# Performance work log

Measured on AMD Instinct MI355X. Metric: run time of the kernel, lower is better.

Reference implementation:

```python
import jax, jax.numpy as jnp
import numpy as np

B, T, C, H, R = 2, 2048, 2048, 16, 8
D = C // H  # head_dim = 128


def _rope_cache(seq_len, dim, theta=10000.0):
    pos = jnp.arange(seq_len, dtype=jnp.float32)[:, None]            # [T,1]
    idx = jnp.arange(0, dim, 2, dtype=jnp.float32)                   # [D/2]
    freqs = 1.0 / (theta ** (idx / dim))
    ang = pos * freqs                                                # [T, D/2]
    return jnp.cos(ang), jnp.sin(ang)


def setup_inputs() -> dict:
    key = jax.random.key(0)
    ks = jax.random.split(key, 16)
    s = 0.02
    inp = {"x": jax.random.normal(ks[0], (B, T, C), dtype=jnp.float32)}
    i = 1
    for nm in ("q", "k", "v", "p"):
        inp[f"{nm}_w"] = jax.random.normal(ks[i], (C, C), dtype=jnp.float32) * s; i += 1
        inp[f"{nm}_b"] = jnp.zeros((C,), dtype=jnp.float32)
        inp[f"{nm}_A"] = jax.random.normal(ks[i], (C, R), dtype=jnp.float32) * s; i += 1
        inp[f"{nm}_B"] = jax.random.normal(ks[i], (R, C), dtype=jnp.float32) * s; i += 1
    cos, sin = _rope_cache(T, D)
    inp["cos"] = cos
    inp["sin"] = sin
    inp["mask"] = jnp.tril(jnp.ones((T, T), dtype=bool))  # causal SDPA mask
    inp["use_lora"] = 1
    return inp


def _lora_linear(x, w, b, A, Bm, use_lora):
    # base GEMM + bias, plus low-rank adapter x @ A @ B (intended path)
    out = x @ w.T + b
    if use_lora:
        out = out + (x @ A) @ Bm
    return out


def _apply_rope(x, cos, sin):
    # x: [B,H,T,D]; cos/sin: [T, D/2] broadcast over batch & heads
    x1 = x[..., ::2]
    x2 = x[..., 1::2]
    y = jnp.stack((x1 * cos - x2 * sin, x1 * sin + x2 * cos), axis=-1)
    return y.reshape(x.shape)


def reference(x, q_w, q_b, q_A, q_B, k_w, k_b, k_A, k_B,
              v_w, v_b, v_A, v_B, p_w, p_b, p_A, p_B,
              cos, sin, mask, use_lora):
    Bsz, Tl, Cd = x.shape
    q = _lora_linear(x, q_w, q_b, q_A, q_B, use_lora).reshape(Bsz, Tl, H, D).transpose(0, 2, 1, 3)
    k = _lora_linear(x, k_w, k_b, k_A, k_B, use_lora).reshape(Bsz, Tl, H, D).transpose(0, 2, 1, 3)
    v = _lora_linear(x, v_w, v_b, v_A, v_B, use_lora).reshape(Bsz, Tl, H, D).transpose(0, 2, 1, 3)
    q = _apply_rope(q, cos, sin)
    k = _apply_rope(k, cos, sin)
    # scaled dot-product attention with boolean mask (True = attend)
    scale = 1.0 / jnp.sqrt(jnp.asarray(D, dtype=x.dtype))
    scores = jnp.einsum('bhqd,bhkd->bhqk', q, k) * scale          # [B,H,T,T]
    neg = jnp.asarray(jnp.finfo(scores.dtype).min, dtype=scores.dtype)
    scores = jnp.where(mask, scores, neg)
    attn = jax.nn.softmax(scores, axis=-1)
    out = jnp.einsum('bhqk,bhkd->bhqd', attn, v)                  # [B,H,T,D]
    y = out.transpose(0, 2, 1, 3).reshape(Bsz, Tl, Cd)
    return _lora_linear(y, p_w, p_b, p_A, p_B, use_lora)
```

## Files before the change

### kernel.cpp

```cpp
#include <hip/hip_runtime.h>

typedef _Float16 f16;
typedef _Float16 f16x4 __attribute__((ext_vector_type(4)));
typedef _Float16 f16x8 __attribute__((ext_vector_type(8)));
typedef __fp16 hf2 __attribute__((ext_vector_type(2)));
typedef float f32x4 __attribute__((ext_vector_type(4)));

#define DEV static __device__ __forceinline__

DEV void gl_lds16(const void* g, void* l) {
  __builtin_amdgcn_global_load_lds(
      (const __attribute__((address_space(1))) void*)g,
      (__attribute__((address_space(3))) void*)l, 16, 0, 0);
}

DEV uint pkrtz(float a, float b) {
  hf2 h = __builtin_amdgcn_cvt_pkrtz(a, b);
  return __builtin_bit_cast(uint, h);
}

DEV f32x4 MFMA(f16x8 a, f16x8 b, f32x4 c) {
  return __builtin_amdgcn_mfma_f32_16x16x32_f16(a, b, c, 0, 0, 0);
}

__global__ void cast_f16_kernel(const float* __restrict__ x,
                                const float* __restrict__ w0,
                                const float* __restrict__ w1,
                                const float* __restrict__ w2,
                                const float* __restrict__ w3,
                                f16* __restrict__ xb, f16* __restrict__ b0,
                                f16* __restrict__ b1, f16* __restrict__ b2,
                                f16* __restrict__ b3) {
  const int total4 = (8388608 + 4 * 4194304) / 4;
  for (int i = blockIdx.x * blockDim.x + threadIdx.x; i < total4;
       i += gridDim.x * blockDim.x) {
    int e = i << 2;
    const float* s; f16* d; int off;
    if (e < 8388608)        { s = x;  d = xb; off = e; }
    else if (e < 12582912)  { s = w0; d = b0; off = e - 8388608; }
    else if (e < 16777216)  { s = w1; d = b1; off = e - 12582912; }
    else if (e < 20971520)  { s = w2; d = b2; off = e - 16777216; }
    else                    { s = w3; d = b3; off = e - 20971520; }
    float4 v = *(const float4*)(s + off);
    f16x4 hv = {(f16)v.x, (f16)v.y, (f16)v.z, (f16)v.w};
    *(f16x4*)(d + off) = hv;
  }
}

__global__ __launch_bounds__(256) void lora_x_kernel(
    const float* __restrict__ x, const float* __restrict__ Aq,
    const float* __restrict__ Ak, const float* __restrict__ Av,
    float* __restrict__ la) {
  const int wave = threadIdx.x >> 6, lane = threadIdx.x & 63;
  const int m = blockIdx.x * 4 + wave;
  const float* xrow = x + (size_t)m * 2048;
  const float* As[3] = {Aq, Ak, Av};
  float acc[3][8] = {};
  for (int i = 0; i < 32; ++i) {
    int k = i * 64 + lane;
    float xv = xrow[k];
#pragma unroll
    for (int nm = 0; nm < 3; ++nm) {
      const float4* ap = (const float4*)(As[nm] + (size_t)k * 8);
      float4 a0 = ap[0], a1 = ap[1];
      acc[nm][0] += xv * a0.x; acc[nm][1] += xv * a0.y;
      acc[nm][2] += xv * a0.z; acc[nm][3] += xv * a0.w;
      acc[nm][4] += xv * a1.x; acc[nm][5] += xv * a1.y;
      acc[nm][6] += xv * a1.z; acc[nm][7] += xv * a1.w;
    }
  }
#pragma unroll
  for (int nm = 0; nm < 3; ++nm)
#pragma unroll
    for (int r = 0; r < 8; ++r) {
      float v = acc[nm][r];
#pragma unroll
      for (int off = 1; off < 64; off <<= 1) v += __shfl_xor(v, off);
      acc[nm][r] = v;
    }
  if (lane == 0) {
#pragma unroll
    for (int nm = 0; nm < 3; ++nm)
#pragma unroll
      for (int r = 0; r < 8; ++r)
        la[nm * 32768 + (size_t)m * 8 + r] = acc[nm][r];
  }
}

__global__ __launch_bounds__(256) void lora_p_kernel(
    const f16* __restrict__ y, const float* __restrict__ Ap,
    float* __restrict__ lap) {
  const int wave = threadIdx.x >> 6, lane = threadIdx.x & 63;
  const int m = blockIdx.x * 4 + wave;
  const f16* yrow = y + (size_t)m * 2048;
  float acc[8] = {};
  for (int i = 0; i < 4; ++i) {
    int k0 = i * 512 + lane * 8;
    f16x8 yv = *(const f16x8*)(yrow + k0);
#pragma unroll
    for (int j = 0; j < 8; ++j) {
      float xv = (float)yv[j];
      const float4* ap = (const float4*)(Ap + (size_t)(k0 + j) * 8);
      float4 a0 = ap[0], a1 = ap[1];
      acc[0] += xv * a0.x; acc[1] += xv * a0.y;
      acc[2] += xv * a0.z; acc[3] += xv * a0.w;
      acc[4] += xv * a1.x; acc[5] += xv * a1.y;
      acc[6] += xv * a1.z; acc[7] += xv * a1.w;
    }
  }
#pragma unroll
  for (int r = 0; r < 8; ++r) {
    float v = acc[r];
#pragma unroll
    for (int off = 1; off < 64; off <<= 1) v += __shfl_xor(v, off);
    acc[r] = v;
  }
  if (lane == 0) {
#pragma unroll
    for (int r = 0; r < 8; ++r) lap[(size_t)m * 8 + r] = acc[r];
  }
}

template <int MODE>
__global__ __launch_bounds__(512, 1) void gemm_kernel(
    const f16* __restrict__ A, const f16* __restrict__ Bw,
    const float* __restrict__ bias, const float* __restrict__ la,
    const float* __restrict__ Bm, const int* __restrict__ use_lora,
    const float* __restrict__ cosT, const float* __restrict__ sinT,
    void* __restrict__ out) {
  extern __shared__ char smem[];
  const int tid = threadIdx.x;
  const int wave = tid >> 6, lane = tid & 63;
  const int lr = lane & 15, lg = lane >> 4;
  const int bm = (int)blockIdx.x >> 3, bn = (int)blockIdx.x & 7;
  const int m0 = bm << 7, n0 = bn << 8;
  const int wr = wave >> 2, wc = wave & 3;

  const char* Ab = (const char*)A;
  const char* Bb = (const char*)Bw;

  auto stageA = [&](int kt, int bsel, int sw) {
    uint base = (uint)sw * 8192u + (uint)wave * 1024u;
    uint idx = base + (uint)lane * 16u;
    uint row = idx >> 7, cb = idx & 127u;
    uint c = cb ^ ((row & 7u) << 4);
    gl_lds16(Ab + (size_t)(m0 + row) * 4096 + (size_t)kt * 128 + c,
             smem + bsel * 49152 + base);
  };
  auto stageB = [&](int kt, int bsel, int sw) {
    uint base = (uint)sw * 8192u + (uint)wave * 1024u;
    uint idx = base + (uint)lane * 16u;
    uint row = idx >> 7, cb = idx & 127u;
    uint c = cb ^ ((row & 7u) << 4);
    gl_lds16(Bb + (size_t)(n0 + row) * 4096 + (size_t)kt * 128 + c,
             smem + bsel * 49152 + 16384 + base);
  };
  auto rdA = [&](int bsel, int ks, int mi) -> f16x8 {
    int row = wr * 64 + mi * 16 + lr;
    int c = (ks * 64 + lg * 16) ^ ((row & 7) << 4);
    return *(const f16x8*)(smem + bsel * 49152 + row * 128 + c);
  };
  auto rdB = [&](int bsel, int ks, int ni) -> f16x8 {
    int row = wc * 64 + ni * 16 + lr;
    int c = (ks * 64 + lg * 16) ^ ((row & 7) << 4);
    return *(const f16x8*)(smem + bsel * 49152 + 16384 + row * 128 + c);
  };

  f32x4 acc[4][4] = {};

#pragma unroll
  for (int sw = 0; sw < 2; ++sw) stageA(0, 0, sw);
#pragma unroll
  for (int sw = 0; sw < 4; ++sw) stageB(0, 0, sw);
#pragma unroll
  for (int sw = 0; sw < 2; ++sw) stageA(1, 1, sw);
#pragma unroll
  for (int sw = 0; sw < 4; ++sw) stageB(1, 1, sw);

  for (int kt = 0; kt < 32; ++kt) {
    const int cur = kt % 3;
    const int nxt = (kt + 2) % 3;
    const bool st = (kt + 2 < 32);
    if (kt == 31) asm volatile("s_waitcnt vmcnt(0)" ::: "memory");
    else         asm volatile("s_waitcnt vmcnt(6)" ::: "memory");
    __builtin_amdgcn_s_barrier();

    f16x8 a0, a1, a2, a3, b0, b1;
    a0 = rdA(cur, 0, 0); a1 = rdA(cur, 0, 1);
    a2 = rdA(cur, 0, 2); a3 = rdA(cur, 0, 3);
    b0 = rdB(cur, 0, 0); b1 = rdB(cur, 0, 1);
    if (st) { stageA(kt + 2, nxt, 0); stageA(kt + 2, nxt, 1); }
    __builtin_amdgcn_s_setprio(1);
    acc[0][0] = MFMA(a0, b0, acc[0][0]); acc[1][0] = MFMA(a1, b0, acc[1][0]);
    acc[2][0] = MFMA(a2, b0, acc[2][0]); acc[3][0] = MFMA(a3, b0, acc[3][0]);
    acc[0][1] = MFMA(a0, b1, acc[0][1]); acc[1][1] = MFMA(a1, b1, acc[1][1]);
    acc[2][1] = MFMA(a2, b1, acc[2][1]); acc[3][1] = MFMA(a3, b1, acc[3][1]);
    __builtin_amdgcn_s_setprio(0);
    __builtin_amdgcn_s_barrier();

    b0 = rdB(cur, 0, 2); b1 = rdB(cur, 0, 3);
    if (st) { stageB(kt + 2, nxt, 0); stageB(kt + 2, nxt, 1); }
    __builtin_amdgcn_s_setprio(1);
    acc[0][2] = MFMA(a0, b0, acc[0][2]); acc[1][2] = MFMA(a1, b0, acc[1][2]);
    acc[2][2] = MFMA(a2, b0, acc[2][2]); acc[3][2] = MFMA(a3, b0, acc[3][2]);
    acc[0][3] = MFMA(a0, b1, acc[0][3]); acc[1][3] = MFMA(a1, b1, acc[1][3]);
    acc[2][3] = MFMA(a2, b1, acc[2][3]); acc[3][3] = MFMA(a3, b1, acc[3][3]);
    __builtin_amdgcn_s_setprio(0);
    __builtin_amdgcn_s_barrier();

    a0 = rdA(cur, 1, 0); a1 = rdA(cur, 1, 1);
    a2 = rdA(cur, 1, 2); a3 = rdA(cur, 1, 3);
    b0 = rdB(cur, 1, 0); b1 = rdB(cur, 1, 1);
    if (st) { stageB(kt + 2, nxt, 2); stageB(kt + 2, nxt, 3); }
    __builtin_amdgcn_s_setprio(1);
    acc[0][0] = MFMA(a0, b0, acc[0][0]); acc[1][0] = MFMA(a1, b0, acc[1][0]);
    acc[2][0] = MFMA(a2, b0, acc[2][0]); acc[3][0] = MFMA(a3, b0, acc[3][0]);
    acc[0][1] = MFMA(a0, b1, acc[0][1]); acc[1][1] = MFMA(a1, b1, acc[1][1]);
    acc[2][1] = MFMA(a2, b1, acc[2][1]); acc[3][1] = MFMA(a3, b1, acc[3][1]);
    __builtin_amdgcn_s_setprio(0);
    __builtin_amdgcn_s_barrier();

    b0 = rdB(cur, 1, 2); b1 = rdB(cur, 1, 3);
    __builtin_amdgcn_s_setprio(1);
    acc[0][2] = MFMA(a0, b0, acc[0][2]); acc[1][2] = MFMA(a1, b0, acc[1][2]);
    acc[2][2] = MFMA(a2, b0, acc[2][2]); acc[3][2] = MFMA(a3, b0, acc[3][2]);
    acc[0][3] = MFMA(a0, b1, acc[0][3]); acc[1][3] = MFMA(a1, b1, acc[1][3]);
    acc[2][3] = MFMA(a2, b1, acc[2][3]); acc[3][3] = MFMA(a3, b1, acc[3][3]);
    __builtin_amdgcn_s_setprio(0);
  }
  __builtin_amdgcn_s_barrier();

  const int ul = use_lora[0];
  float bv[4], bml[4][8];
#pragma unroll
  for (int ni = 0; ni < 4; ++ni) {
    int n = n0 + wc * 64 + ni * 16 + lr;
    bv[ni] = bias[n];
    if (ul) {
#pragma unroll
      for (int r = 0; r < 8; ++r) bml[ni][r] = Bm[r * 2048 + n];
    }
  }

#pragma unroll
  for (int mi = 0; mi < 4; ++mi) {
    const int mbase = m0 + wr * 64 + mi * 16 + lg * 4;
    float lar[4][8];
    if (ul) {
#pragma unroll
      for (int rg = 0; rg < 4; ++rg) {
        const float4* lp = (const float4*)(la + (size_t)(mbase + rg) * 8);
        float4 l0 = lp[0], l1 = lp[1];
        lar[rg][0] = l0.x; lar[rg][1] = l0.y; lar[rg][2] = l0.z; lar[rg][3] = l0.w;
        lar[rg][4] = l1.x; lar[rg][5] = l1.y; lar[rg][6] = l1.z; lar[rg][7] = l1.w;
      }
    }
#pragma unroll
    for (int ni = 0; ni < 4; ++ni) {
      const int n = n0 + wc * 64 + ni * 16 + lr;
#pragma unroll
      for (int rg = 0; rg < 4; ++rg) {
        float v = acc[mi][ni][rg] + bv[ni];
        if (ul) {
#pragma unroll
          for (int r = 0; r < 8; ++r) v += lar[rg][r] * bml[ni][r];
        }
        const int lrow = wr * 64 + mi * 16 + lg * 4 + rg;
        if (MODE == 0) {
          float pv = __shfl_xor(v, 1);
          const int t = (mbase + rg) & 2047;
          const int d = n & 127;
          const int ci = t * 64 + (d >> 1);
          float cs = cosT[ci], sn = sinT[ci];
          float res = ((lane & 1) == 0) ? (v * cs - pv * sn)
                                        : (pv * sn + v * cs);
          int cbyte = ((wc * 64 + ni * 16 + lr) * 2) ^ ((lrow & 7) << 4);
          *(f16*)(smem + lrow * 512 + cbyte) = (f16)res;
        } else if (MODE == 1) {
          int cbyte = ((wc * 64 + ni * 16 + lr) * 2) ^ ((lrow & 7) << 4);
          *(f16*)(smem + lrow * 512 + cbyte) = (f16)v;
        } else {
          ((float*)out)[(size_t)(mbase + rg) * 2048 + n] = v;
        }
      }
    }
  }

  if (MODE < 2) {
    __builtin_amdgcn_s_barrier();
#pragma unroll
    for (int p = 0; p < 8; ++p) {
      int s = p * 8192 + tid * 16;
      int row = s >> 9, cb = s & 511;
      int c = cb ^ ((row & 7) << 4);
      uint4 val = *(const uint4*)(smem + row * 512 + c);
      if (MODE == 0) {
        const long b_ = (m0 + row) >> 11;
        const int tb = (m0 + row) & 2047;
        const int head = 2 * bn + (cb >> 8);
        char* dst = (char*)out + ((b_ * 16 + head) * 2048 + tb) * 256 + (cb & 255);
        *(uint4*)dst = val;
      } else {
        char* dst = (char*)out + ((long)(m0 + row) * 2048 + bn * 256) * 2 + cb;
        *(uint4*)dst = val;
      }
    }
  }
}

__global__ void transpose_v_kernel(const ushort* __restrict__ vbi,
                                   ushort* __restrict__ vto) {
  __shared__ ushort tile[32][33];
  const int t0 = blockIdx.x << 5;
  const int d0 = blockIdx.y << 5;
  const int bh = blockIdx.z;
  const int b = bh >> 4, h = bh & 15;
  const int tx = threadIdx.x, ty = threadIdx.y;
  const ushort* src = vbi + ((size_t)(b * 2048 + t0)) * 2048 + h * 128 + d0;
#pragma unroll
  for (int i = 0; i < 4; ++i)
    tile[ty + 8 * i][tx] = src[(size_t)(ty + 8 * i) * 2048 + tx];
  __syncthreads();
  ushort* dst = vto + ((size_t)bh * 128 + d0) * 2048 + t0;
#pragma unroll
  for (int i = 0; i < 4; ++i)
    dst[(size_t)(ty + 8 * i) * 2048 + tx] = tile[tx][ty + 8 * i];
}

__global__ __launch_bounds__(256, 2) void attn_kernel(
    const f16* __restrict__ qr, const f16* __restrict__ kr,
    const f16* __restrict__ vt, f16* __restrict__ y) {
  extern __shared__ char smem[];
  const int tid = threadIdx.x, wave = tid >> 6, lane = tid & 63;
  const int lr = lane & 15, lg = lane >> 4;
  const int qt = 15 - (int)blockIdx.x;
  const int q0 = qt << 7;
  const int h = blockIdx.y, b = blockIdx.z;
  const long bh = b * 16 + h;
  const int nt = 2 * qt + 2;

  const char* kbase = (const char*)kr + bh * 2048 * 256;
  const char* vbase = (const char*)vt + bh * 128 * 4096;

  f16x8 qf[2][4];
#pragma unroll
  for (int g = 0; g < 2; ++g) {
    const char* qb =
        (const char*)qr + (bh * 2048 + q0 + wave * 32 + g * 16 + lr) * 256;
#pragma unroll
    for (int ks = 0; ks < 4; ++ks)
      qf[g][ks] = *(const f16x8*)(qb + ks * 64 + lg * 16);
  }

  f32x4 o[2][8] = {};
  float mrow[2] = {-3e38f, -3e38f};
  float lsum[2] = {0.f, 0.f};
  const float SC2 = 0.12752551286084103f;

  auto STAGE = [&](int kv0, int bsel) {
    char* Ks = smem + bsel * 32768;
    char* Vs = Ks + 16384;
#pragma unroll
    for (int r = 0; r < 4; ++r) {
      uint s = (uint)(wave * 4 + r) * 1024 + (uint)lane * 16;
      uint rowk = s >> 8, ck = (s & 255u) ^ ((rowk & 7u) << 4);
      gl_lds16(kbase + (size_t)(kv0 + rowk) * 256 + ck,
               Ks + (wave * 4 + r) * 1024);
      uint rowv = s >> 7, cv = (s & 127u) ^ ((rowv & 7u) << 4);
      gl_lds16(vbase + (size_t)rowv * 4096 + kv0 * 2 + cv,
               Vs + (wave * 4 + r) * 1024);
    }
  };

  STAGE(0, 0);
  __syncthreads();

  for (int kt = 0; kt < nt; ++kt) {
    const int kv0 = kt << 6;
    if (kt + 1 < nt) STAGE((kt + 1) << 6, (kt + 1) & 1);
    const char* Ks = smem + (kt & 1) * 32768;
    const char* Vs = Ks + 16384;

    if (kv0 <= q0 + wave * 32 + 31) {
      f32x4 sa[2][4] = {};
      __builtin_amdgcn_s_setprio(1);
#pragma unroll
      for (int ks = 0; ks < 4; ++ks)
#pragma unroll
        for (int n = 0; n < 4; ++n) {
          int row = n * 16 + lr;
          int c = (ks * 64 + lg * 16) ^ ((row & 7) << 4);
          f16x8 kf = *(const f16x8*)(Ks + row * 256 + c);
          sa[0][n] = MFMA(kf, qf[0][ks], sa[0][n]);
          sa[1][n] = MFMA(kf, qf[1][ks], sa[1][n]);
        }
      __builtin_amdgcn_s_setprio(0);

      f16x8 pf[2][2];
#pragma unroll
      for (int g = 0; g < 2; ++g) {
        const int qgbase = q0 + wave * 32 + g * 16;
        float L[16];
        float pm = -3e38f;
        const bool dm = (kv0 + 63 > qgbase);
#pragma unroll
        for (int n = 0; n < 4; ++n)
#pragma unroll
          for (int rg = 0; rg < 4; ++rg) {
            float Lv = sa[g][n][rg] * SC2;
            if (dm && (kv0 + n * 16 + lg * 4 + rg > qgbase + lr)) Lv = -3e37f;
            L[n * 4 + rg] = Lv;
            pm = fmaxf(pm, Lv);
          }
        pm = fmaxf(pm, __shfl_xor(pm, 16));
        pm = fmaxf(pm, __shfl_xor(pm, 32));
        if (!__all(pm - mrow[g] <= 8.f)) {
          float mn = fmaxf(mrow[g], pm);
          float alpha = exp2f(mrow[g] - mn);
          mrow[g] = mn;
          lsum[g] *= alpha;
#pragma unroll
          for (int dt = 0; dt < 8; ++dt)
#pragma unroll
            for (int rg = 0; rg < 4; ++rg) o[g][dt][rg] *= alpha;
        }
        const float mn = mrow[g];
        float ps = 0.f;
#pragma unroll
        for (int i = 0; i < 16; ++i) {
          float p = exp2f(L[i] - mn);
          L[i] = p;
          ps += p;
        }
        ps += __shfl_xor(ps, 16);
        ps += __shfl_xor(ps, 32);
        lsum[g] += ps;

#pragma unroll
        for (int ks2 = 0; ks2 < 2; ++ks2) {
          uint w0 = pkrtz(L[8 * ks2 + 0], L[8 * ks2 + 1]);
          uint w1 = pkrtz(L[8 * ks2 + 2], L[8 * ks2 + 3]);
          uint w2 = pkrtz(L[8 * ks2 + 4], L[8 * ks2 + 5]);
          uint w3 = pkrtz(L[8 * ks2 + 6], L[8 * ks2 + 7]);
          int src1 = ((lg & 1) << 5) + lr;
          int src2 = src1 + 16;
          uint a0 = __shfl((int)w0, src1), a1 = __shfl((int)w1, src1);
          uint a2 = __shfl((int)w2, src1), a3 = __shfl((int)w3, src1);
          uint b0 = __shfl((int)w0, src2), b1 = __shfl((int)w1, src2);
          uint b2 = __shfl((int)w2, src2), b3 = __shfl((int)w3, src2);
          const bool hi = (lg >> 1) != 0;
          uint4 uu;
          uu.x = hi ? a2 : a0;
          uu.y = hi ? a3 : a1;
          uu.z = hi ? b2 : b0;
          uu.w = hi ? b3 : b1;
          pf[g][ks2] = __builtin_bit_cast(f16x8, uu);
        }
      }

#pragma unroll
      for (int ks2 = 0; ks2 < 2; ++ks2) {
        __builtin_amdgcn_s_setprio(1);
#pragma unroll
        for (int dt = 0; dt < 8; ++dt) {
          int drow = dt * 16 + lr;
          int c = (ks2 * 64 + lg * 16) ^ ((drow & 7) << 4);
          f16x8 vf = *(const f16x8*)(Vs + drow * 128 + c);
          o[0][dt] = MFMA(vf, pf[0][ks2], o[0][dt]);
          o[1][dt] = MFMA(vf, pf[1][ks2], o[1][dt]);
        }
        __builtin_amdgcn_s_setprio(0);
      }
    }
    __syncthreads();
  }

#pragma unroll
  for (int g = 0; g < 2; ++g) {
    const float inv = 1.f / lsum[g];
    const int row = wave * 32 + g * 16 + lr;
#pragma unroll
    for (int dt = 0; dt < 8; ++dt) {
      uint lo = pkrtz(o[g][dt][0] * inv, o[g][dt][1] * inv);
      uint hi2 = pkrtz(o[g][dt][2] * inv, o[g][dt][3] * inv);
      int c = (dt * 32 + lg * 8) ^ ((row & 7) << 4);
      uint2 w;
      w.x = lo;
      w.y = hi2;
      *(uint2*)(smem + row * 256 + c) = w;
    }
  }
  __syncthreads();
#pragma unroll
  for (int p = 0; p < 8; ++p) {
    int s = p * 4096 + tid * 16;
    int row = s >> 8, cb = s & 255;
    int c = cb ^ ((row & 7) << 4);
    char* dst =
        (char*)y + ((long)(b * 2048 + q0 + row) * 2048 + h * 128) * 2 + cb;
    *(uint4*)dst = *(const uint4*)(smem + row * 256 + c);
  }
}

extern "C" void kernel_launch(void* const* d_in, const int* in_sizes, int n_in,
                              void* d_out, int out_size, void* d_ws,
                              size_t ws_size, hipStream_t stream) {
  (void)in_sizes; (void)n_in; (void)out_size; (void)ws_size;
  const float* x   = (const float*)d_in[0];
  const float* q_w = (const float*)d_in[1];
  const float* q_b = (const float*)d_in[2];
  const float* q_A = (const float*)d_in[3];
  const float* q_B = (const float*)d_in[4];
  const float* k_w = (const float*)d_in[5];
  const float* k_b = (const float*)d_in[6];
  const float* k_A = (const float*)d_in[7];
  const float* k_B = (const float*)d_in[8];
  const float* v_w = (const float*)d_in[9];
  const float* v_b = (const float*)d_in[10];
  const float* v_A = (const float*)d_in[11];
  const float* v_B = (const float*)d_in[12];
  const float* p_w = (const float*)d_in[13];
  const float* p_b = (const float*)d_in[14];
  const float* p_A = (const float*)d_in[15];
  const float* p_B = (const float*)d_in[16];
  const float* cosT = (const float*)d_in[17];
  const float* sinT = (const float*)d_in[18];
  const int* use_lora = (const int*)d_in[20];

  char* ws = (char*)d_ws;
  f16* xb  = (f16*)(ws);
  f16* wqb = (f16*)(ws + 16777216);
  f16* wkb = (f16*)(ws + 25165824);
  f16* wvb = (f16*)(ws + 33554432);
  f16* wpb = (f16*)(ws + 41943040);
  float* la = (float*)(ws + 50331648);
  f16* qr  = (f16*)(ws + 50855936);
  f16* kr  = (f16*)(ws + 67633152);
  f16* vb  = (f16*)(ws + 84410368);
  f16* vt  = (f16*)(ws);
  f16* y   = vb;
  float* lap = la + 98304;

  cast_f16_kernel<<<dim3(2048), dim3(256), 0, stream>>>(
      x, q_w, k_w, v_w, p_w, xb, wqb, wkb, wvb, wpb);
  lora_x_kernel<<<dim3(1024), dim3(256), 0, stream>>>(x, q_A, k_A, v_A, la);
  gemm_kernel<0><<<dim3(256), dim3(512), 147456, stream>>>(
      xb, wqb, q_b, la, q_B, use_lora, cosT, sinT, (void*)qr);
  gemm_kernel<0><<<dim3(256), dim3(512), 147456, stream>>>(
      xb, wkb, k_b, la + 32768, k_B, use_lora, cosT, sinT, (void*)kr);
  gemm_kernel<1><<<dim3(256), dim3(512), 147456, stream>>>(
      xb, wvb, v_b, la + 65536, v_B, use_lora, nullptr, nullptr, (void*)vb);
  transpose_v_kernel<<<dim3(64, 4, 32), dim3(32, 8), 0, stream>>>(
      (const ushort*)vb, (ushort*)vt);
  attn_kernel<<<dim3(16, 16, 2), dim3(256), 65536, stream>>>(qr, kr, vt, y);
  lora_p_kernel<<<dim3(1024), dim3(256), 0, stream>>>(y, p_A, lap);
  gemm_kernel<2><<<dim3(256), dim3(512), 147456, stream>>>(
      y, wpb, p_b, lap, p_B, use_lora, nullptr, nullptr, d_out);
}
```

Measured before the change: 384.1 us.

## Shrink attention query tile to 64 rows, single-buffer LDS, raise occupancy

The attention kernel now gives each block 64 query rows instead of 128, so each wave handles one 16-row group rather than two. K/V staging drops from double-buffered to single-buffered 32KB static LDS, with a sync before and after each load. Launch bounds go from 2 to 4 blocks per SIMD/CU and the grid doubles to 32 query tiles, trading lost prefetch overlap and lower K/V reuse per load for more resident waves and finer causal work balance.

```diff
diff --git a/kernel.cpp b/kernel.cpp
--- a/kernel.cpp
+++ b/kernel.cpp
@@ -327,62 +327,49 @@
     dst[(size_t)(ty + 8 * i) * 2048 + tx] = tile[tx][ty + 8 * i];
 }
 
-__global__ __launch_bounds__(256, 2) void attn_kernel(
+__global__ __launch_bounds__(256, 4) void attn_kernel(
     const f16* __restrict__ qr, const f16* __restrict__ kr,
     const f16* __restrict__ vt, f16* __restrict__ y) {
-  extern __shared__ char smem[];
+  __shared__ char smem[32768];
   const int tid = threadIdx.x, wave = tid >> 6, lane = tid & 63;
   const int lr = lane & 15, lg = lane >> 4;
-  const int qt = 15 - (int)blockIdx.x;
-  const int q0 = qt << 7;
+  const int qt = 31 - (int)blockIdx.x;
+  const int q0 = qt << 6;
   const int h = blockIdx.y, b = blockIdx.z;
   const long bh = b * 16 + h;
-  const int nt = 2 * qt + 2;
+  const int nt = qt + 1;
 
   const char* kbase = (const char*)kr + bh * 2048 * 256;
   const char* vbase = (const char*)vt + bh * 128 * 4096;
 
-  f16x8 qf[2][4];
-#pragma unroll
-  for (int g = 0; g < 2; ++g) {
-    const char* qb =
-        (const char*)qr + (bh * 2048 + q0 + wave * 32 + g * 16 + lr) * 256;
-#pragma unroll
-    for (int ks = 0; ks < 4; ++ks)
-      qf[g][ks] = *(const f16x8*)(qb + ks * 64 + lg * 16);
-  }
-
-  f32x4 o[2][8] = {};
-  float mrow[2] = {-3e38f, -3e38f};
-  float lsum[2] = {0.f, 0.f};
+  const char* qb = (const char*)qr + (bh * 2048 + q0 + wave * 16 + lr) * 256;
+  f16x8 qf[4];
+#pragma unroll
+  for (int ks = 0; ks < 4; ++ks)
+    qf[ks] = *(const f16x8*)(qb + ks * 64 + lg * 16);
+
+  f32x4 o[8] = {};
+  float mrow = -3e38f, lsum = 0.f;
+  const int qwbase = q0 + wave * 16;
   const float SC2 = 0.12752551286084103f;
 
-  auto STAGE = [&](int kv0, int bsel) {
-    char* Ks = smem + bsel * 32768;
-    char* Vs = Ks + 16384;
+  for (int kt = 0; kt < nt; ++kt) {
+    const int kv0 = kt << 6;
+    __syncthreads();
 #pragma unroll
     for (int r = 0; r < 4; ++r) {
       uint s = (uint)(wave * 4 + r) * 1024 + (uint)lane * 16;
       uint rowk = s >> 8, ck = (s & 255u) ^ ((rowk & 7u) << 4);
       gl_lds16(kbase + (size_t)(kv0 + rowk) * 256 + ck,
-               Ks + (wave * 4 + r) * 1024);
+               smem + (wave * 4 + r) * 1024);
       uint rowv = s >> 7, cv = (s & 127u) ^ ((rowv & 7u) << 4);
       gl_lds16(vbase + (size_t)rowv * 4096 + kv0 * 2 + cv,
-               Vs + (wave * 4 + r) * 1024);
-    }
-  };
-
-  STAGE(0, 0);
-  __syncthreads();
-
-  for (int kt = 0; kt < nt; ++kt) {
-    const int kv0 = kt << 6;
-    if (kt + 1 < nt) STAGE((kt + 1) << 6, (kt + 1) & 1);
-    const char* Ks = smem + (kt & 1) * 32768;
-    const char* Vs = Ks + 16384;
-
-    if (kv0 <= q0 + wave * 32 + 31) {
-      f32x4 sa[2][4] = {};
+               smem + 16384 + (wave * 4 + r) * 1024);
+    }
+    __syncthreads();
+
+    if (kv0 <= qwbase + 15) {
+      f32x4 sa[4] = {};
       __builtin_amdgcn_s_setprio(1);
 #pragma unroll
       for (int ks = 0; ks < 4; ++ks)
@@ -390,72 +377,67 @@
         for (int n = 0; n < 4; ++n) {
           int row = n * 16 + lr;
           int c = (ks * 64 + lg * 16) ^ ((row & 7) << 4);
-          f16x8 kf = *(const f16x8*)(Ks + row * 256 + c);
-          sa[0][n] = MFMA(kf, qf[0][ks], sa[0][n]);
-          sa[1][n] = MFMA(kf, qf[1][ks], sa[1][n]);
+          f16x8 kf = *(const f16x8*)(smem + row * 256 + c);
+          sa[n] = MFMA(kf, qf[ks], sa[n]);
         }
       __builtin_amdgcn_s_setprio(0);
 
-      f16x8 pf[2][2];
-#pragma unroll
-      for (int g = 0; g < 2; ++g) {
-        const int qgbase = q0 + wave * 32 + g * 16;
-        float L[16];
-        float pm = -3e38f;
-        const bool dm = (kv0 + 63 > qgbase);
-#pragma unroll
-        for (int n = 0; n < 4; ++n)
-#pragma unroll
-          for (int rg = 0; rg < 4; ++rg) {
-            float Lv = sa[g][n][rg] * SC2;
-            if (dm && (kv0 + n * 16 + lg * 4 + rg > qgbase + lr)) Lv = -3e37f;
-            L[n * 4 + rg] = Lv;
-            pm = fmaxf(pm, Lv);
-          }
-        pm = fmaxf(pm, __shfl_xor(pm, 16));
-        pm = fmaxf(pm, __shfl_xor(pm, 32));
-        if (!__all(pm - mrow[g] <= 8.f)) {
-          float mn = fmaxf(mrow[g], pm);
-          float alpha = exp2f(mrow[g] - mn);
-          mrow[g] = mn;
-          lsum[g] *= alpha;
-#pragma unroll
-          for (int dt = 0; dt < 8; ++dt)
-#pragma unroll
-            for (int rg = 0; rg < 4; ++rg) o[g][dt][rg] *= alpha;
+      float L[16];
+      float pm = -3e38f;
+      const bool dm = (kv0 + 63 > qwbase);
+#pragma unroll
+      for (int n = 0; n < 4; ++n)
+#pragma unroll
+        for (int rg = 0; rg < 4; ++rg) {
+          float Lv = sa[n][rg] * SC2;
+          if (dm && (kv0 + n * 16 + lg * 4 + rg > qwbase + lr)) Lv = -3e37f;
+          L[n * 4 + rg] = Lv;
+          pm = fmaxf(pm, Lv);
         }
-        const float mn = mrow[g];
-        float ps = 0.f;
-#pragma unroll
-        for (int i = 0; i < 16; ++i) {
-          float p = exp2f(L[i] - mn);
-          L[i] = p;
-          ps += p;
-        }
-        ps += __shfl_xor(ps, 16);
-        ps += __shfl_xor(ps, 32);
-        lsum[g] += ps;
-
-#pragma unroll
-        for (int ks2 = 0; ks2 < 2; ++ks2) {
-          uint w0 = pkrtz(L[8 * ks2 + 0], L[8 * ks2 + 1]);
-          uint w1 = pkrtz(L[8 * ks2 + 2], L[8 * ks2 + 3]);
-          uint w2 = pkrtz(L[8 * ks2 + 4], L[8 * ks2 + 5]);
-          uint w3 = pkrtz(L[8 * ks2 + 6], L[8 * ks2 + 7]);
-          int src1 = ((lg & 1) << 5) + lr;
-          int src2 = src1 + 16;
-          uint a0 = __shfl((int)w0, src1), a1 = __shfl((int)w1, src1);
-          uint a2 = __shfl((int)w2, src1), a3 = __shfl((int)w3, src1);
-          uint b0 = __shfl((int)w0, src2), b1 = __shfl((int)w1, src2);
-          uint b2 = __shfl((int)w2, src2), b3 = __shfl((int)w3, src2);
-          const bool hi = (lg >> 1) != 0;
-          uint4 uu;
-          uu.x = hi ? a2 : a0;
-          uu.y = hi ? a3 : a1;
-          uu.z = hi ? b2 : b0;
-          uu.w = hi ? b3 : b1;
-          pf[g][ks2] = __builtin_bit_cast(f16x8, uu);
-        }
+      pm = fmaxf(pm, __shfl_xor(pm, 16));
+      pm = fmaxf(pm, __shfl_xor(pm, 32));
+      if (!__all(pm - mrow <= 8.f)) {
+        float mn = fmaxf(mrow, pm);
+        float alpha = exp2f(mrow - mn);
+        mrow = mn;
+        lsum *= alpha;
+#pragma unroll
+        for (int dt = 0; dt < 8; ++dt)
+#pragma unroll
+          for (int rg = 0; rg < 4; ++rg) o[dt][rg] *= alpha;
+      }
+      const float mn = mrow;
+      float ps = 0.f;
+#pragma unroll
+      for (int i = 0; i < 16; ++i) {
+        float p = exp2f(L[i] - mn);
+        L[i] = p;
+        ps += p;
+      }
+      ps += __shfl_xor(ps, 16);
+      ps += __shfl_xor(ps, 32);
+      lsum += ps;
+
+      f16x8 pf[2];
+#pragma unroll
+      for (int ks2 = 0; ks2 < 2; ++ks2) {
+        uint w0 = pkrtz(L[8 * ks2 + 0], L[8 * ks2 + 1]);
+        uint w1 = pkrtz(L[8 * ks2 + 2], L[8 * ks2 + 3]);
+        uint w2 = pkrtz(L[8 * ks2 + 4], L[8 * ks2 + 5]);
+        uint w3 = pkrtz(L[8 * ks2 + 6], L[8 * ks2 + 7]);
+        int src1 = ((lg & 1) << 5) + lr;
+        int src2 = src1 + 16;
+        uint a0 = __shfl((int)w0, src1), a1 = __shfl((int)w1, src1);
+        uint a2 = __shfl((int)w2, src1), a3 = __shfl((int)w3, src1);
+        uint b0 = __shfl((int)w0, src2), b1 = __shfl((int)w1, src2);
+        uint b2 = __shfl((int)w2, src2), b3 = __shfl((int)w3, src2);
+        const bool hi = (lg >> 1) != 0;
+        uint4 uu;
+        uu.x = hi ? a2 : a0;
+        uu.y = hi ? a3 : a1;
+        uu.z = hi ? b2 : b0;
+        uu.w = hi ? b3 : b1;
+        pf[ks2] = __builtin_bit_cast(f16x8, uu);
       }
 
 #pragma unroll
@@ -465,24 +447,22 @@
         for (int dt = 0; dt < 8; ++dt) {
           int drow = dt * 16 + lr;
           int c = (ks2 * 64 + lg * 16) ^ ((drow & 7) << 4);
-          f16x8 vf = *(const f16x8*)(Vs + drow * 128 + c);
-          o[0][dt] = MFMA(vf, pf[0][ks2], o[0][dt]);
-          o[1][dt] = MFMA(vf, pf[1][ks2], o[1][dt]);
+          f16x8 vf = *(const f16x8*)(smem + 16384 + drow * 128 + c);
+          o[dt] = MFMA(vf, pf[ks2], o[dt]);
         }
         __builtin_amdgcn_s_setprio(0);
       }
     }
-    __syncthreads();
-  }
-
-#pragma unroll
-  for (int g = 0; g < 2; ++g) {
-    const float inv = 1.f / lsum[g];
-    const int row = wave * 32 + g * 16 + lr;
+  }
+
+  __syncthreads();
+  const float inv = 1.f / lsum;
+  {
+    const int row = wave * 16 + lr;
 #pragma unroll
     for (int dt = 0; dt < 8; ++dt) {
-      uint lo = pkrtz(o[g][dt][0] * inv, o[g][dt][1] * inv);
-      uint hi2 = pkrtz(o[g][dt][2] * inv, o[g][dt][3] * inv);
+      uint lo = pkrtz(o[dt][0] * inv, o[dt][1] * inv);
+      uint hi2 = pkrtz(o[dt][2] * inv, o[dt][3] * inv);
       int c = (dt * 32 + lg * 8) ^ ((row & 7) << 4);
       uint2 w;
       w.x = lo;
@@ -492,7 +472,7 @@
   }
   __syncthreads();
 #pragma unroll
-  for (int p = 0; p < 8; ++p) {
+  for (int p = 0; p < 4; ++p) {
     int s = p * 4096 + tid * 16;
     int row = s >> 8, cb = s & 255;
     int c = cb ^ ((row & 7) << 4);
@@ -552,7 +532,7 @@
       xb, wvb, v_b, la + 65536, v_B, use_lora, nullptr, nullptr, (void*)vb);
   transpose_v_kernel<<<dim3(64, 4, 32), dim3(32, 8), 0, stream>>>(
       (const ushort*)vb, (ushort*)vt);
-  attn_kernel<<<dim3(16, 16, 2), dim3(256), 65536, stream>>>(qr, kr, vt, y);
+  attn_kernel<<<dim3(32, 16, 2), dim3(256), 0, stream>>>(qr, kr, vt, y);
   lora_p_kernel<<<dim3(1024), dim3(256), 0, stream>>>(y, p_A, lap);
   gemm_kernel<2><<<dim3(256), dim3(512), 147456, stream>>>(
       y, wpb, p_b, lap, p_B, use_lora, nullptr, nullptr, d_out);
```

Result: slower. 398.8 us (+3.8%).
